# Performance work log

Measured on AMD Instinct MI355X. Metric: run time of the kernel, lower is better.

The kernel has to match this reference:

```python
import jax, jax.numpy as jnp
import numpy as np

EMBED_DIM = 1024
NUM_HEADS = 16
D_K = EMBED_DIM // NUM_HEADS
MAX_SEQ = 2048
BATCH = 2
SEQ = 2048
ROPE_BASE = 10000.0


def build_rope(seq_len, head_dim, base=ROPE_BASE):
    # standard RoPE: inv_freq over half the head dim, cos/sin of shape [seq, head_dim]
    inv_freq = 1.0 / (base ** (jnp.arange(0, head_dim, 2, dtype=jnp.float32) / head_dim))
    t = jnp.arange(seq_len, dtype=jnp.float32)
    freqs = jnp.einsum('s,d->sd', t, inv_freq)              # [S, D/2]
    emb = jnp.concatenate([freqs, freqs], axis=-1)          # [S, D]
    return jnp.cos(emb), jnp.sin(emb)


def rotate_half(x):
    x1, x2 = jnp.split(x, 2, axis=-1)
    return jnp.concatenate([-x2, x1], axis=-1)


def apply_rope(x, cos, sin):
    # x: [B, H, S, D]; cos/sin: [S, D] -> broadcast over batch & heads
    cos = cos[None, None, :, :]
    sin = sin[None, None, :, :]
    return x * cos + rotate_half(x) * sin


def setup_inputs() -> dict:
    key = jax.random.key(0)
    ks = jax.random.split(key, 9)
    scale = 1.0 / np.sqrt(EMBED_DIM)
    x = jax.random.normal(ks[0], (BATCH, SEQ, EMBED_DIM), dtype=jnp.float32)
    # causal boolean mask, broadcastable to [B, H, S, S]
    mask = jnp.tril(jnp.ones((SEQ, SEQ), dtype=bool))[None, None, :, :]
    cos, sin = build_rope(MAX_SEQ, D_K)
    Wq = jax.random.normal(ks[1], (EMBED_DIM, EMBED_DIM), jnp.float32) * scale
    bq = jnp.zeros((EMBED_DIM,), jnp.float32)
    Wk = jax.random.normal(ks[2], (EMBED_DIM, EMBED_DIM), jnp.float32) * scale
    bk = jnp.zeros((EMBED_DIM,), jnp.float32)
    Wv = jax.random.normal(ks[3], (EMBED_DIM, EMBED_DIM), jnp.float32) * scale
    bv = jnp.zeros((EMBED_DIM,), jnp.float32)
    Wo = jax.random.normal(ks[4], (EMBED_DIM, EMBED_DIM), jnp.float32) * scale
    bo = jnp.zeros((EMBED_DIM,), jnp.float32)
    return {'x': x, 'mask': mask, 'cos': cos, 'sin': sin,
            'Wq': Wq, 'bq': bq, 'Wk': Wk, 'bk': bk, 'Wv': Wv, 'bv': bv,
            'Wo': Wo, 'bo': bo}


def reference(x, mask, cos, sin, Wq, bq, Wk, bk, Wv, bv, Wo, bo):
    B, S, E = x.shape
    H, D = NUM_HEADS, D_K
    # nn.Linear: y = x @ W^T + b
    q = (x @ Wq.T + bq).reshape(B, S, H, D).transpose(0, 2, 1, 3)  # [B,H,S,D]
    k = (x @ Wk.T + bk).reshape(B, S, H, D).transpose(0, 2, 1, 3)
    v = (x @ Wv.T + bv).reshape(B, S, H, D).transpose(0, 2, 1, 3)
    q = apply_rope(q, cos[:S], sin[:S])
    k = apply_rope(k, cos[:S], sin[:S])
    scores = jnp.einsum('bhqd,bhkd->bhqk', q, k) / jnp.sqrt(jnp.float32(D))
    scores = jnp.where(mask, scores, -jnp.inf)
    attn = jax.nn.softmax(scores, axis=-1)
    out = jnp.einsum('bhqk,bhkd->bhqd', attn, v)
    out = out.transpose(0, 2, 1, 3).reshape(B, S, E)
    return out @ Wo.T + bo
```

## Files before the change

### kernel.cpp

```cpp
#include <hip/hip_runtime.h>
#include <hip/hip_bf16.h>
#include <cfloat>
#include <math.h>

#define EMBED 1024
#define NHEADS 16
#define DK 64
#define SEQL 2048
#define BATCH 2
#define NTOK 4096


typedef __bf16 bf16x8 __attribute__((ext_vector_type(8)));
typedef float floatx4 __attribute__((ext_vector_type(4)));

__device__ __forceinline__ unsigned short f2bf(float f) {
    union { __hip_bfloat16 b; unsigned short u; } c;
    c.b = __float2bfloat16(f);
    return c.u;
}

__global__ __launch_bounds__(256) void convert_pack(
    const float* __restrict__ x,  const float* __restrict__ Wq,
    const float* __restrict__ Wk, const float* __restrict__ Wv,
    const float* __restrict__ Wo,
    unsigned short* __restrict__ xb, unsigned short* __restrict__ Wqkv,
    unsigned short* __restrict__ Wob)
{
    const int XG = 1048576, WG = 262144;
    int g = blockIdx.x * 256 + threadIdx.x;
    const float4* s; ushort4* d;
    if (g < XG)               { s = (const float4*)x  + g;                d = (ushort4*)xb   + g; }
    else if (g < XG + WG)     { s = (const float4*)Wq + (g - XG);         d = (ushort4*)Wqkv + (g - XG); }
    else if (g < XG + 2 * WG) { s = (const float4*)Wk + (g - XG - WG);    d = (ushort4*)Wqkv + (g - XG); }
    else if (g < XG + 3 * WG) { s = (const float4*)Wv + (g - XG - 2*WG);  d = (ushort4*)Wqkv + (g - XG); }
    else                      { s = (const float4*)Wo + (g - XG - 3*WG);  d = (ushort4*)Wob  + (g - XG - 3*WG); }
    float4 v = *s;
    *d = (ushort4){f2bf(v.x), f2bf(v.y), f2bf(v.z), f2bf(v.w)};
}

#define QP 40

__global__ __launch_bounds__(256) void qkv_gemm(
    const unsigned short* __restrict__ xb, const unsigned short* __restrict__ Wqkv,
    const float* __restrict__ bq, const float* __restrict__ bk, const float* __restrict__ bv,
    const float* __restrict__ cosT, const float* __restrict__ sinT,
    unsigned short* __restrict__ Qg, unsigned short* __restrict__ Kg,
    unsigned short* __restrict__ Vt)
{
    __shared__ __align__(16) unsigned short SM[2 * 128 * QP];
    unsigned short* As = SM;
    unsigned short* Bs = SM + 128 * QP;

    const int t = threadIdx.x, lane = t & 63, wave = t >> 6;
    const int quad = lane >> 4, lrow = lane & 15;
    const int m0 = blockIdx.y * 128;
    const int n0 = blockIdx.x * 128;
    const int mw = (wave & 1) * 64, nw = (wave >> 1) * 64;
    const int r = t >> 1, kc = (t & 1) * 16;

    floatx4 acc[4][4];
    #pragma unroll
    for (int i = 0; i < 4; i++)
        #pragma unroll
        for (int j = 0; j < 4; j++) acc[i][j] = (floatx4){0.f,0.f,0.f,0.f};

    for (int k0 = 0; k0 < EMBED; k0 += 32) {
        const unsigned short* ap = xb   + (size_t)(m0 + r) * EMBED + k0 + kc;
        const unsigned short* bp = Wqkv + (size_t)(n0 + r) * EMBED + k0 + kc;
        uint4 a0 = *(const uint4*)ap, a1 = *(const uint4*)(ap + 8);
        uint4 b0 = *(const uint4*)bp, b1 = *(const uint4*)(bp + 8);
        __syncthreads();
        *(uint4*)&As[r * QP + kc]     = a0;  *(uint4*)&As[r * QP + kc + 8] = a1;
        *(uint4*)&Bs[r * QP + kc]     = b0;  *(uint4*)&Bs[r * QP + kc + 8] = b1;
        __syncthreads();

        bf16x8 af[4], bfB[4];
        #pragma unroll
        for (int i = 0; i < 4; i++)
            af[i] = *reinterpret_cast<const bf16x8*>(&As[(mw + i * 16 + lrow) * QP + quad * 8]);
        #pragma unroll
        for (int j = 0; j < 4; j++)
            bfB[j] = *reinterpret_cast<const bf16x8*>(&Bs[(nw + j * 16 + lrow) * QP + quad * 8]);
        #pragma unroll
        for (int i = 0; i < 4; i++)
            #pragma unroll
            for (int j = 0; j < 4; j++)
                acc[i][j] = __builtin_amdgcn_mfma_f32_16x16x32_bf16(af[i], bfB[j], acc[i][j], 0, 0, 0);
    }

    const int mat  = n0 >> 10;
    const int nloc = n0 & 1023;
    const int bb   = m0 >> 11;
    const int s0   = m0 & (SEQL - 1);

    for (int hn = 0; hn < 2; hn++) {
        const int h = (nloc >> 6) + hn;
        __syncthreads();
        if (mat == 2) {
            unsigned short* T2 = SM;
            if ((wave >> 1) == hn) {
                #pragma unroll
                for (int j = 0; j < 4; j++) {
                    int d = j * 16 + lrow;
                    float bvv = bv[nloc + hn * 64 + d];
                    #pragma unroll
                    for (int i = 0; i < 4; i++) {
                        int tok = mw + i * 16 + quad * 4;
                        *(ushort4*)&T2[d * 136 + tok] = (ushort4){
                            f2bf(acc[i][j][0] + bvv), f2bf(acc[i][j][1] + bvv),
                            f2bf(acc[i][j][2] + bvv), f2bf(acc[i][j][3] + bvv)};
                    }
                }
            }
            __syncthreads();
            int d = t >> 2, tg = (t & 3) * 32;
            unsigned short* dst = Vt + ((size_t)(bb * NHEADS + h) * DK + d) * SEQL + s0 + tg;
            #pragma unroll
            for (int c = 0; c < 32; c += 8)
                *(uint4*)(dst + c) = *(const uint4*)&T2[d * 136 + tg + c];
        } else {
            unsigned short* T = SM;
            const float* bias = (mat == 0) ? bq : bk;
            if ((wave >> 1) == hn) {
                #pragma unroll
                for (int j = 0; j < 4; j++) {
                    int d = j * 16 + lrow;
                    float bvv = bias[nloc + hn * 64 + d];
                    #pragma unroll
                    for (int i = 0; i < 4; i++)
                        #pragma unroll
                        for (int rg = 0; rg < 4; rg++)
                            T[(mw + i * 16 + quad * 4 + rg) * 72 + d] = f2bf(acc[i][j][rg] + bvv);
                }
            }
            __syncthreads();
            int tok = t >> 1, dh = (t & 1) * 32;
            int s = s0 + tok;
            float sgn = dh ? 1.0f : -1.0f;
            unsigned short* dst = ((mat == 0) ? Qg : Kg)
                + ((size_t)(bb * NHEADS + h) * SEQL + s) * DK + dh;
            #pragma unroll
            for (int c = 0; c < 32; c += 8) {
                bf16x8 own = *reinterpret_cast<const bf16x8*>(&T[tok * 72 + dh + c]);
                bf16x8 par = *reinterpret_cast<const bf16x8*>(&T[tok * 72 + (dh ^ 32) + c]);
                float4 c0 = *(const float4*)(cosT + s * DK + dh + c);
                float4 c1 = *(const float4*)(cosT + s * DK + dh + c + 4);
                float4 s0v = *(const float4*)(sinT + s * DK + dh + c);
                float4 s1v = *(const float4*)(sinT + s * DK + dh + c + 4);
                float cv[8] = {c0.x,c0.y,c0.z,c0.w,c1.x,c1.y,c1.z,c1.w};
                float sv[8] = {s0v.x,s0v.y,s0v.z,s0v.w,s1v.x,s1v.y,s1v.z,s1v.w};
                unsigned short o[8];
                #pragma unroll
                for (int e = 0; e < 8; e++)
                    o[e] = f2bf((float)own[e] * cv[e] + sgn * (float)par[e] * sv[e]);
                *(uint4*)(dst + c) = *(const uint4*)o;
            }
        }
    }
}

#define KP 72

__global__ __launch_bounds__(256) void attn_mfma(
    const unsigned short* __restrict__ Qg, const unsigned short* __restrict__ Kg,
    const unsigned short* __restrict__ Vt, unsigned short* __restrict__ CTX)
{
    __shared__ __align__(16) unsigned short Ks[64 * KP];
    __shared__ __align__(16) unsigned short Vs[64 * KP];
    __shared__ __align__(16) unsigned short Ps[64 * KP];

    const int p = blockIdx.x;
    const int h = blockIdx.y, b = blockIdx.z;
    const int qtL = p, qtH = (SEQL / 64 - 1) - p;
    const int t = threadIdx.x;
    const int lane = t & 63, w = t >> 6;
    const int quad = lane >> 4, lrow = lane & 15;
    const int q0L = qtL * 64, q0H = qtH * 64;

    const unsigned short* Qh = Qg + (size_t)(b * NHEADS + h) * SEQL * DK;
    const unsigned short* Kh = Kg + (size_t)(b * NHEADS + h) * SEQL * DK;
    const unsigned short* Vh = Vt + (size_t)(b * NHEADS + h) * DK * SEQL;

    bf16x8 aqL[2], aqH[2];
    #pragma unroll
    for (int ks = 0; ks < 2; ks++) {
        aqL[ks] = *(const bf16x8*)(Qh + (size_t)(q0L + w * 16 + lrow) * DK + quad * 8 + ks * 32);
        aqH[ks] = *(const bf16x8*)(Qh + (size_t)(q0H + w * 16 + lrow) * DK + quad * 8 + ks * 32);
    }

    floatx4 ofL[4], ofH[4];
    float lL[4] = {0,0,0,0}, lH[4] = {0,0,0,0};
    #pragma unroll
    for (int jd = 0; jd < 4; jd++) { ofL[jd] = (floatx4){0,0,0,0}; ofH[jd] = (floatx4){0,0,0,0}; }

    unsigned short* Pw = Ps + w * 16 * KP;

    const int r0 = t >> 3, c8 = (t & 7) * 8;
    uint4 pk0, pk1, pv0, pv1;
    auto pref = [&](int k0) {
        pk0 = *(const uint4*)(Kh + (size_t)(k0 + r0) * DK + c8);
        pk1 = *(const uint4*)(Kh + (size_t)(k0 + r0 + 32) * DK + c8);
        pv0 = *(const uint4*)(Vh + (size_t)r0 * SEQL + k0 + c8);
        pv1 = *(const uint4*)(Vh + (size_t)(r0 + 32) * SEQL + k0 + c8);
    };
    pref(0);

    for (int kt = 0; kt <= qtH; kt++) {
        const int k0 = kt * 64;
        __syncthreads();
        *(uint4*)&Ks[r0 * KP + c8]        = pk0;
        *(uint4*)&Ks[(r0 + 32) * KP + c8] = pk1;
        *(uint4*)&Vs[r0 * KP + c8]        = pv0;
        *(uint4*)&Vs[(r0 + 32) * KP + c8] = pv1;
        __syncthreads();
        if (kt < qtH) pref(k0 + 64);

        {
            floatx4 sc[4];
            #pragma unroll
            for (int j = 0; j < 4; j++) sc[j] = (floatx4){0,0,0,0};
            #pragma unroll
            for (int ks = 0; ks < 2; ks++)
                #pragma unroll
                for (int j = 0; j < 4; j++) {
                    bf16x8 kb = *reinterpret_cast<const bf16x8*>(&Ks[(j * 16 + lrow) * KP + quad * 8 + ks * 32]);
                    sc[j] = __builtin_amdgcn_mfma_f32_16x16x32_bf16(aqH[ks], kb, sc[j], 0, 0, 0);
                }
            const bool diag = (kt == qtH);
            #pragma unroll
            for (int rg = 0; rg < 4; rg++) {
                int row = q0H + w * 16 + quad * 4 + rg;
                float lacc = 0.f;
                #pragma unroll
                for (int j = 0; j < 4; j++) {
                    float pval = __expf(sc[j][rg] * 0.125f);
                    if (diag && (k0 + j * 16 + lrow) > row) pval = 0.f;
                    Pw[(quad * 4 + rg) * KP + j * 16 + lrow] = f2bf(pval);
                    lacc += pval;
                }
                lH[rg] += lacc;
            }
            #pragma unroll
            for (int ks = 0; ks < 2; ks++) {
                bf16x8 pa = *reinterpret_cast<const bf16x8*>(&Pw[lrow * KP + quad * 8 + ks * 32]);
                #pragma unroll
                for (int jd = 0; jd < 4; jd++) {
                    bf16x8 vb = *reinterpret_cast<const bf16x8*>(&Vs[(jd * 16 + lrow) * KP + quad * 8 + ks * 32]);
                    ofH[jd] = __builtin_amdgcn_mfma_f32_16x16x32_bf16(pa, vb, ofH[jd], 0, 0, 0);
                }
            }
        }
        if (kt <= qtL) {
            floatx4 sc[4];
            #pragma unroll
            for (int j = 0; j < 4; j++) sc[j] = (floatx4){0,0,0,0};
            #pragma unroll
            for (int ks = 0; ks < 2; ks++)
                #pragma unroll
                for (int j = 0; j < 4; j++) {
                    bf16x8 kb = *reinterpret_cast<const bf16x8*>(&Ks[(j * 16 + lrow) * KP + quad * 8 + ks * 32]);
                    sc[j] = __builtin_amdgcn_mfma_f32_16x16x32_bf16(aqL[ks], kb, sc[j], 0, 0, 0);
                }
            const bool diag = (kt == qtL);
            #pragma unroll
            for (int rg = 0; rg < 4; rg++) {
                int row = q0L + w * 16 + quad * 4 + rg;
                float lacc = 0.f;
                #pragma unroll
                for (int j = 0; j < 4; j++) {
                    float pval = __expf(sc[j][rg] * 0.125f);
                    if (diag && (k0 + j * 16 + lrow) > row) pval = 0.f;
                    Pw[(quad * 4 + rg) * KP + j * 16 + lrow] = f2bf(pval);
                    lacc += pval;
                }
                lL[rg] += lacc;
            }
            #pragma unroll
            for (int ks = 0; ks < 2; ks++) {
                bf16x8 pa = *reinterpret_cast<const bf16x8*>(&Pw[lrow * KP + quad * 8 + ks * 32]);
                #pragma unroll
                for (int jd = 0; jd < 4; jd++) {
                    bf16x8 vb = *reinterpret_cast<const bf16x8*>(&Vs[(jd * 16 + lrow) * KP + quad * 8 + ks * 32]);
                    ofL[jd] = __builtin_amdgcn_mfma_f32_16x16x32_bf16(pa, vb, ofL[jd], 0, 0, 0);
                }
            }
        }
    }

    #pragma unroll
    for (int rg = 0; rg < 4; rg++) {
        float lv = lH[rg];
        #pragma unroll
        for (int off = 1; off < 16; off <<= 1) lv += __shfl_xor(lv, off);
        float inv = 1.0f / lv;
        int row = q0H + w * 16 + quad * 4 + rg;
        unsigned short* Cr = CTX + ((size_t)(b * NHEADS + h) * SEQL + row) * DK;
        #pragma unroll
        for (int jd = 0; jd < 4; jd++) Cr[jd * 16 + lrow] = f2bf(ofH[jd][rg] * inv);

        lv = lL[rg];
        #pragma unroll
        for (int off = 1; off < 16; off <<= 1) lv += __shfl_xor(lv, off);
        inv = 1.0f / lv;
        row = q0L + w * 16 + quad * 4 + rg;
        Cr = CTX + ((size_t)(b * NHEADS + h) * SEQL + row) * DK;
        #pragma unroll
        for (int jd = 0; jd < 4; jd++) Cr[jd * 16 + lrow] = f2bf(ofL[jd][rg] * inv);
    }
}

#define LSTR 40

__global__ __launch_bounds__(256) void o_gemm(
    const unsigned short* __restrict__ Ag,
    const unsigned short* __restrict__ Bg,
    const float* __restrict__ bias, float* __restrict__ C)
{
    __shared__ __align__(16) unsigned short As[64 * LSTR];
    __shared__ __align__(16) unsigned short Bs[64 * LSTR];

    const int t = threadIdx.x, lane = t & 63, wave = t >> 6;
    const int quad = lane >> 4, lrow = lane & 15;
    const int m0 = blockIdx.y * 64, n0 = blockIdx.x * 64;
    const int mw = (wave & 1) * 32, nw = (wave >> 1) * 32;
    const int r = t >> 2, kc = (t & 3) * 8;

    floatx4 acc[2][2];
    #pragma unroll
    for (int i = 0; i < 2; i++)
        #pragma unroll
        for (int j = 0; j < 2; j++) acc[i][j] = (floatx4){0,0,0,0};

    for (int k0 = 0; k0 < EMBED; k0 += 32) {
        int tok = m0 + r, k = k0 + kc;
        size_t aaddr = ((size_t)((tok >> 11) * NHEADS + (k >> 6)) * SEQL + (tok & (SEQL - 1))) * DK + (k & 63);
        uint4 a0 = *(const uint4*)(Ag + aaddr);
        uint4 b0 = *(const uint4*)(Bg + (size_t)(n0 + r) * EMBED + k0 + kc);
        __syncthreads();
        *(uint4*)&As[r * LSTR + kc] = a0;
        *(uint4*)&Bs[r * LSTR + kc] = b0;
        __syncthreads();

        bf16x8 af[2], bfB[2];
        #pragma unroll
        for (int i = 0; i < 2; i++)
            af[i] = *reinterpret_cast<const bf16x8*>(&As[(mw + i * 16 + lrow) * LSTR + quad * 8]);
        #pragma unroll
        for (int j = 0; j < 2; j++)
            bfB[j] = *reinterpret_cast<const bf16x8*>(&Bs[(nw + j * 16 + lrow) * LSTR + quad * 8]);
        #pragma unroll
        for (int i = 0; i < 2; i++)
            #pragma unroll
            for (int j = 0; j < 2; j++)
                acc[i][j] = __builtin_amdgcn_mfma_f32_16x16x32_bf16(af[i], bfB[j], acc[i][j], 0, 0, 0);
    }

    #pragma unroll
    for (int i = 0; i < 2; i++)
        #pragma unroll
        for (int rg = 0; rg < 4; rg++) {
            int row_g = m0 + mw + i * 16 + quad * 4 + rg;
            #pragma unroll
            for (int j = 0; j < 2; j++) {
                int col_g = n0 + nw + j * 16 + lrow;
                C[(size_t)row_g * EMBED + col_g] = acc[i][j][rg] + bias[col_g];
            }
        }
}

extern "C" void kernel_launch(void* const* d_in, const int* in_sizes, int n_in,
                              void* d_out, int out_size, void* d_ws, size_t ws_size,
                              hipStream_t stream) {
    const float* x    = (const float*)d_in[0];
    const float* cosT = (const float*)d_in[2];
    const float* sinT = (const float*)d_in[3];
    const float* Wq = (const float*)d_in[4];  const float* bq = (const float*)d_in[5];
    const float* Wk = (const float*)d_in[6];  const float* bk = (const float*)d_in[7];
    const float* Wv = (const float*)d_in[8];  const float* bv = (const float*)d_in[9];
    const float* Wo = (const float*)d_in[10]; const float* bo = (const float*)d_in[11];

    const size_t MB = 1024 * 1024;
    char* ws = (char*)d_ws;
    unsigned short* xb   = (unsigned short*)(ws);
    unsigned short* Wqkv = (unsigned short*)(ws +  8 * MB);
    unsigned short* Wob  = (unsigned short*)(ws + 14 * MB);
    unsigned short* Qg   = (unsigned short*)(ws + 16 * MB);
    unsigned short* Kg   = (unsigned short*)(ws + 24 * MB);
    unsigned short* Vt   = (unsigned short*)(ws + 32 * MB);
    unsigned short* CTXb = (unsigned short*)(ws + 40 * MB);

    convert_pack<<<8192, 256, 0, stream>>>(x, Wq, Wk, Wv, Wo, xb, Wqkv, Wob);

    dim3 qkv_grid(3 * EMBED / 128, NTOK / 128);
    qkv_gemm<<<qkv_grid, 256, 0, stream>>>(xb, Wqkv, bq, bk, bv, cosT, sinT, Qg, Kg, Vt);

    dim3 attn_grid(SEQL / 128, NHEADS, BATCH);
    attn_mfma<<<attn_grid, 256, 0, stream>>>(Qg, Kg, Vt, CTXb);

    dim3 o_grid(EMBED / 64, NTOK / 64);
    o_gemm<<<o_grid, 256, 0, stream>>>(CTXb, Wob, bo, (float*)d_out);
}
```

Measured before the change: 263.3 us.

## Use direct global-to-LDS async loads in QKV and output GEMMs, enlarge o_gemm tiles

Replaces register-staged global loads plus LDS stores in both GEMMs with global_load_lds 16-byte transfers that write straight into shared memory, using an unpadded stride of 32. The output projection GEMM also moves from 64x64 to 128x128 tiles with a 4x4 MFMA fragment per wave, which improves data reuse but cuts the block count to 256. The unpadded LDS layout may cause bank conflicts on fragment reads, and the smaller o_gemm grid lowers occupancy.

After: 255.7 us. 2.9% less time.

```diff
diff --git a/kernel.cpp b/kernel.cpp
--- a/kernel.cpp
+++ b/kernel.cpp
@@ -18,6 +18,13 @@
     union { __hip_bfloat16 b; unsigned short u; } c;
     c.b = __float2bfloat16(f);
     return c.u;
+}
+
+__device__ __forceinline__ void async16(void* lds, const void* g) {
+    __builtin_amdgcn_global_load_lds(
+        (const __attribute__((address_space(1))) unsigned int*)g,
+        (__attribute__((address_space(3))) unsigned int*)lds,
+        16, 0, 0);
 }
 
 __global__ __launch_bounds__(256) void convert_pack(
@@ -39,8 +46,6 @@
     *d = (ushort4){f2bf(v.x), f2bf(v.y), f2bf(v.z), f2bf(v.w)};
 }
 
-#define QP 40
-
 __global__ __launch_bounds__(256) void qkv_gemm(
     const unsigned short* __restrict__ xb, const unsigned short* __restrict__ Wqkv,
     const float* __restrict__ bq, const float* __restrict__ bk, const float* __restrict__ bv,
@@ -48,16 +53,17 @@
     unsigned short* __restrict__ Qg, unsigned short* __restrict__ Kg,
     unsigned short* __restrict__ Vt)
 {
-    __shared__ __align__(16) unsigned short SM[2 * 128 * QP];
+    __shared__ __align__(16) unsigned short SM[9216];
     unsigned short* As = SM;
-    unsigned short* Bs = SM + 128 * QP;
+    unsigned short* Bs = SM + 4096;
 
     const int t = threadIdx.x, lane = t & 63, wave = t >> 6;
     const int quad = lane >> 4, lrow = lane & 15;
     const int m0 = blockIdx.y * 128;
     const int n0 = blockIdx.x * 128;
     const int mw = (wave & 1) * 64, nw = (wave >> 1) * 64;
-    const int r = t >> 1, kc = (t & 1) * 16;
+    const int srow = lane >> 2;
+    const int scol = (lane & 3) * 8;
 
     floatx4 acc[4][4];
     #pragma unroll
@@ -65,23 +71,24 @@
         #pragma unroll
         for (int j = 0; j < 4; j++) acc[i][j] = (floatx4){0.f,0.f,0.f,0.f};
 
+    const unsigned short* Ab = xb   + (size_t)(m0 + wave * 32 + srow) * EMBED + scol;
+    const unsigned short* Bb = Wqkv + (size_t)(n0 + wave * 32 + srow) * EMBED + scol;
+
     for (int k0 = 0; k0 < EMBED; k0 += 32) {
-        const unsigned short* ap = xb   + (size_t)(m0 + r) * EMBED + k0 + kc;
-        const unsigned short* bp = Wqkv + (size_t)(n0 + r) * EMBED + k0 + kc;
-        uint4 a0 = *(const uint4*)ap, a1 = *(const uint4*)(ap + 8);
-        uint4 b0 = *(const uint4*)bp, b1 = *(const uint4*)(bp + 8);
-        __syncthreads();
-        *(uint4*)&As[r * QP + kc]     = a0;  *(uint4*)&As[r * QP + kc + 8] = a1;
-        *(uint4*)&Bs[r * QP + kc]     = b0;  *(uint4*)&Bs[r * QP + kc + 8] = b1;
+        __syncthreads();
+        async16(&As[wave * 1024],       Ab + k0);
+        async16(&As[wave * 1024 + 512], Ab + 16 * EMBED + k0);
+        async16(&Bs[wave * 1024],       Bb + k0);
+        async16(&Bs[wave * 1024 + 512], Bb + 16 * EMBED + k0);
         __syncthreads();
 
         bf16x8 af[4], bfB[4];
         #pragma unroll
         for (int i = 0; i < 4; i++)
-            af[i] = *reinterpret_cast<const bf16x8*>(&As[(mw + i * 16 + lrow) * QP + quad * 8]);
+            af[i] = *reinterpret_cast<const bf16x8*>(&As[(mw + i * 16 + lrow) * 32 + quad * 8]);
         #pragma unroll
         for (int j = 0; j < 4; j++)
-            bfB[j] = *reinterpret_cast<const bf16x8*>(&Bs[(nw + j * 16 + lrow) * QP + quad * 8]);
+            bfB[j] = *reinterpret_cast<const bf16x8*>(&Bs[(nw + j * 16 + lrow) * 32 + quad * 8]);
         #pragma unroll
         for (int i = 0; i < 4; i++)
             #pragma unroll
@@ -310,59 +317,63 @@
     }
 }
 
-#define LSTR 40
-
 __global__ __launch_bounds__(256) void o_gemm(
     const unsigned short* __restrict__ Ag,
     const unsigned short* __restrict__ Bg,
     const float* __restrict__ bias, float* __restrict__ C)
 {
-    __shared__ __align__(16) unsigned short As[64 * LSTR];
-    __shared__ __align__(16) unsigned short Bs[64 * LSTR];
+    __shared__ __align__(16) unsigned short As[128 * 32];
+    __shared__ __align__(16) unsigned short Bs[128 * 32];
 
     const int t = threadIdx.x, lane = t & 63, wave = t >> 6;
     const int quad = lane >> 4, lrow = lane & 15;
-    const int m0 = blockIdx.y * 64, n0 = blockIdx.x * 64;
-    const int mw = (wave & 1) * 32, nw = (wave >> 1) * 32;
-    const int r = t >> 2, kc = (t & 3) * 8;
-
-    floatx4 acc[2][2];
-    #pragma unroll
-    for (int i = 0; i < 2; i++)
-        #pragma unroll
-        for (int j = 0; j < 2; j++) acc[i][j] = (floatx4){0,0,0,0};
+    const int m0 = blockIdx.y * 128, n0 = blockIdx.x * 128;
+    const int mw = (wave & 1) * 64, nw = (wave >> 1) * 64;
+    const int srow = lane >> 2;
+    const int scol = (lane & 3) * 8;
+
+    floatx4 acc[4][4];
+    #pragma unroll
+    for (int i = 0; i < 4; i++)
+        #pragma unroll
+        for (int j = 0; j < 4; j++) acc[i][j] = (floatx4){0.f,0.f,0.f,0.f};
+
+    const int tokA0 = m0 + wave * 32 + srow;
+    const unsigned short* Bb = Bg + (size_t)(n0 + wave * 32 + srow) * EMBED + scol;
 
     for (int k0 = 0; k0 < EMBED; k0 += 32) {
-        int tok = m0 + r, k = k0 + kc;
-        size_t aaddr = ((size_t)((tok >> 11) * NHEADS + (k >> 6)) * SEQL + (tok & (SEQL - 1))) * DK + (k & 63);
-        uint4 a0 = *(const uint4*)(Ag + aaddr);
-        uint4 b0 = *(const uint4*)(Bg + (size_t)(n0 + r) * EMBED + k0 + kc);
-        __syncthreads();
-        *(uint4*)&As[r * LSTR + kc] = a0;
-        *(uint4*)&Bs[r * LSTR + kc] = b0;
-        __syncthreads();
-
-        bf16x8 af[2], bfB[2];
-        #pragma unroll
-        for (int i = 0; i < 2; i++)
-            af[i] = *reinterpret_cast<const bf16x8*>(&As[(mw + i * 16 + lrow) * LSTR + quad * 8]);
-        #pragma unroll
-        for (int j = 0; j < 2; j++)
-            bfB[j] = *reinterpret_cast<const bf16x8*>(&Bs[(nw + j * 16 + lrow) * LSTR + quad * 8]);
-        #pragma unroll
-        for (int i = 0; i < 2; i++)
-            #pragma unroll
-            for (int j = 0; j < 2; j++)
+        int k = k0 + scol;
+        size_t a0 = ((size_t)((tokA0 >> 11) * NHEADS + (k >> 6)) * SEQL + (tokA0 & (SEQL - 1))) * DK + (k & 63);
+        int tokA1 = tokA0 + 16;
+        size_t a1 = ((size_t)((tokA1 >> 11) * NHEADS + (k >> 6)) * SEQL + (tokA1 & (SEQL - 1))) * DK + (k & 63);
+        __syncthreads();
+        async16(&As[wave * 1024],       Ag + a0);
+        async16(&As[wave * 1024 + 512], Ag + a1);
+        async16(&Bs[wave * 1024],       Bb + k0);
+        async16(&Bs[wave * 1024 + 512], Bb + 16 * EMBED + k0);
+        __syncthreads();
+
+        bf16x8 af[4], bfB[4];
+        #pragma unroll
+        for (int i = 0; i < 4; i++)
+            af[i] = *reinterpret_cast<const bf16x8*>(&As[(mw + i * 16 + lrow) * 32 + quad * 8]);
+        #pragma unroll
+        for (int j = 0; j < 4; j++)
+            bfB[j] = *reinterpret_cast<const bf16x8*>(&Bs[(nw + j * 16 + lrow) * 32 + quad * 8]);
+        #pragma unroll
+        for (int i = 0; i < 4; i++)
+            #pragma unroll
+            for (int j = 0; j < 4; j++)
                 acc[i][j] = __builtin_amdgcn_mfma_f32_16x16x32_bf16(af[i], bfB[j], acc[i][j], 0, 0, 0);
     }
 
     #pragma unroll
-    for (int i = 0; i < 2; i++)
+    for (int i = 0; i < 4; i++)
         #pragma unroll
         for (int rg = 0; rg < 4; rg++) {
             int row_g = m0 + mw + i * 16 + quad * 4 + rg;
             #pragma unroll
-            for (int j = 0; j < 2; j++) {
+            for (int j = 0; j < 4; j++) {
                 int col_g = n0 + nw + j * 16 + lrow;
                 C[(size_t)row_g * EMBED + col_g] = acc[i][j][rg] + bias[col_g];
             }
@@ -398,6 +409,6 @@
     dim3 attn_grid(SEQL / 128, NHEADS, BATCH);
     attn_mfma<<<attn_grid, 256, 0, stream>>>(Qg, Kg, Vt, CTXb);
 
-    dim3 o_grid(EMBED / 64, NTOK / 64);
+    dim3 o_grid(EMBED / 128, NTOK / 128);
     o_gemm<<<o_grid, 256, 0, stream>>>(CTXb, Wob, bo, (float*)d_out);
 }
```
